# Kernel optimization log

Hardware: AMD Instinct MI355X
Metric: run time of the kernel (lower is better)

The kernel has to match this reference:

```python
import jax, jax.numpy as jnp
import numpy as np

B, T, NG, NP, DV = 256, 100, 4096, 512, 2


def setup_inputs() -> dict:
    key = jax.random.key(0)
    k = jax.random.split(key, 6)
    v = jax.random.normal(k[0], (B, T, DV), dtype=jnp.float32) * 0.1
    P0 = jax.random.uniform(k[1], (B, NP), dtype=jnp.float32)
    # Dense kernels (glorot-ish scale); recurrent kernel uniform(-0.02, 0.02) per the module
    W_enc = jax.random.normal(k[2], (NP, NG), dtype=jnp.float32) / np.sqrt(NP)
    W_in = jax.random.normal(k[3], (DV, NG), dtype=jnp.float32) / np.sqrt(DV)
    W_rec = (jax.random.uniform(k[4], (NG, NG), dtype=jnp.float32) * 2.0 - 1.0) * 0.02
    W_dec = jax.random.normal(k[5], (NG, NP), dtype=jnp.float32) / np.sqrt(NG)
    return {"v": v, "P0": P0, "W_enc": W_enc, "W_in": W_in, "W_rec": W_rec, "W_dec": W_dec}


def reference(v, P0, W_enc, W_in, W_rec, W_dec):
    # encoder: init hidden state from place-cell code P0  -> [B, Ng]
    h0 = P0 @ W_enc
    # Precompute input projection for all timesteps: [B, T, Ng] -> scan over T
    xW = jnp.einsum('btd,dg->btg', v, W_in)
    xW_t = jnp.swapaxes(xW, 0, 1)  # [T, B, Ng]

    def step(h, x):
        h_new = jax.nn.relu(x + h @ W_rec)
        return h_new, h_new

    _, g = jax.lax.scan(step, h0, xW_t)      # g: [T, B, Ng]
    g = jnp.swapaxes(g, 0, 1)                # [B, T, Ng]
    place_preds = jnp.einsum('btg,gp->btp', g, W_dec)  # [B, T, Np]
    return place_preds
```

## Files before the change

### kernel.cpp

```cpp
#include <hip/hip_runtime.h>
#include <hip/hip_bf16.h>

typedef __attribute__((ext_vector_type(8))) short bf16x8;
typedef __attribute__((ext_vector_type(4))) float f32x4;

#define MFMA __builtin_amdgcn_mfma_f32_16x16x32_bf16

__device__ __forceinline__ short f2bf(float f) {
    union { __hip_bfloat16 h; short s; } u;
    u.h = __float2bfloat16(f);
    return u.s;
}

__device__ __forceinline__ void gld_lds16(const void* g, void* l) {
    auto gp = (const __attribute__((address_space(1))) void*)(g);
    auto lp = (__attribute__((address_space(3))) void*)(l);
    __builtin_amdgcn_global_load_lds(gp, lp, 16, 0, 0);
}

__global__ __launch_bounds__(64) void cvt_tile(const float* __restrict__ in,
                                               __hip_bfloat16* __restrict__ out, int C) {
    const int cd32 = C >> 5;
    const int tile = blockIdx.x;
    const int r16 = tile / cd32, c32 = tile - r16 * cd32;
    const int l = threadIdx.x;
    const int row = (r16 << 4) + (l & 15);
    const int c0 = (c32 << 5) + ((l >> 4) << 3);
    const float* src = in + (size_t)row * C + c0;
    short o[8];
#pragma unroll
    for (int j = 0; j < 8; ++j) o[j] = f2bf(src[j]);
    *(bf16x8*)((char*)out + (size_t)tile * 1024 + (l << 4)) = *(bf16x8*)o;
}

__global__ __launch_bounds__(256) void tcvt256(const float* __restrict__ in,
                                               __hip_bfloat16* __restrict__ out,
                                               int N, int K) {
    __shared__ float tile[64][65];
    const int r0 = blockIdx.x << 6;
    const int c0 = blockIdx.y << 6;
    const int tid = threadIdx.x;
    const int row = tid >> 2, cq = tid & 3;
#pragma unroll
    for (int it = 0; it < 4; ++it) {
        int c4 = cq + (it << 2);
        float4 vv = *(const float4*)(in + (size_t)(r0 + row) * N + c0 + (c4 << 2));
        tile[row][(c4 << 2) + 0] = vv.x;
        tile[row][(c4 << 2) + 1] = vv.y;
        tile[row][(c4 << 2) + 2] = vv.z;
        tile[row][(c4 << 2) + 3] = vv.w;
    }
    __syncthreads();
    const int kd32 = K >> 5;
#pragma unroll
    for (int half = 0; half < 2; ++half) {
        int slot = tid + (half << 8);
        int ti = slot >> 6, l = slot & 63;
        int ci = ti & 3, ri = ti >> 2;
        short o[8];
#pragma unroll
        for (int j = 0; j < 8; ++j)
            o[j] = f2bf(tile[(ri << 5) + ((l >> 4) << 3) + j][(ci << 4) + (l & 15)]);
        size_t tidx = (size_t)((c0 >> 4) + ci) * kd32 + (r0 >> 5) + ri;
        *(bf16x8*)((char*)out + tidx * 1024 + (l << 4)) = *(bf16x8*)o;
    }
}

template <int MODE, int NW, int KC>
__global__ __launch_bounds__(NW * 64) void gemm_r(const __hip_bfloat16* __restrict__ A,
                                                  const __hip_bfloat16* __restrict__ B,
                                                  void* __restrict__ outp,
                                                  const float* __restrict__ v,
                                                  const float* __restrict__ Wi, int t) {
    constexpr int KD32 = KC * NW;
    __shared__ __align__(16) char lds[NW * 16384];
    const int id = blockIdx.x;
    const int xcd = id & 7, j = id >> 3;
    const int bn = (xcd << 3) + (j & 7);
    const int bm = j >> 3;
    const int tid = threadIdx.x, wv = tid >> 6, lane = tid & 63;
    char* myl = lds + (wv << 14);
    const int kw0 = wv * KC;
    const int bm4 = bm << 2, bn4 = bn << 2;

    constexpr size_t FSTR = (size_t)KD32 << 10;
    const char* pA = (const char*)A + (((size_t)(bm4 * KD32 + kw0)) << 10) + (lane << 4);
    const char* pB = (const char*)B + (((size_t)(bn4 * KD32 + kw0)) << 10) + (lane << 4);

    f32x4 acc[4][4] = {};
    bf16x8 A00, A01, A02, A03, A10, A11, A12, A13,
           A20, A21, A22, A23, A30, A31, A32, A33;
    bf16x8 B00, B01, B02, B03, B10, B11, B12, B13,
           B20, B21, B22, B23, B30, B31, B32, B33;

#define LOADG(S, KI)                                       \
    do {                                                   \
        const char* pa_ = pA + ((size_t)(KI) << 10);       \
        const char* pb_ = pB + ((size_t)(KI) << 10);       \
        A##S##0 = *(const bf16x8*)(pa_);                   \
        A##S##1 = *(const bf16x8*)(pa_ + FSTR);            \
        A##S##2 = *(const bf16x8*)(pa_ + 2 * FSTR);        \
        A##S##3 = *(const bf16x8*)(pa_ + 3 * FSTR);        \
        B##S##0 = *(const bf16x8*)(pb_);                   \
        B##S##1 = *(const bf16x8*)(pb_ + FSTR);            \
        B##S##2 = *(const bf16x8*)(pb_ + 2 * FSTR);        \
        B##S##3 = *(const bf16x8*)(pb_ + 3 * FSTR);        \
    } while (0)

#define COMPUTE(S)                                             \
    do {                                                       \
        acc[0][0] = MFMA(A##S##0, B##S##0, acc[0][0], 0, 0, 0);\
        acc[0][1] = MFMA(A##S##0, B##S##1, acc[0][1], 0, 0, 0);\
        acc[0][2] = MFMA(A##S##0, B##S##2, acc[0][2], 0, 0, 0);\
        acc[0][3] = MFMA(A##S##0, B##S##3, acc[0][3], 0, 0, 0);\
        acc[1][0] = MFMA(A##S##1, B##S##0, acc[1][0], 0, 0, 0);\
        acc[1][1] = MFMA(A##S##1, B##S##1, acc[1][1], 0, 0, 0);\
        acc[1][2] = MFMA(A##S##1, B##S##2, acc[1][2], 0, 0, 0);\
        acc[1][3] = MFMA(A##S##1, B##S##3, acc[1][3], 0, 0, 0);\
        acc[2][0] = MFMA(A##S##2, B##S##0, acc[2][0], 0, 0, 0);\
        acc[2][1] = MFMA(A##S##2, B##S##1, acc[2][1], 0, 0, 0);\
        acc[2][2] = MFMA(A##S##2, B##S##2, acc[2][2], 0, 0, 0);\
        acc[2][3] = MFMA(A##S##2, B##S##3, acc[2][3], 0, 0, 0);\
        acc[3][0] = MFMA(A##S##3, B##S##0, acc[3][0], 0, 0, 0);\
        acc[3][1] = MFMA(A##S##3, B##S##1, acc[3][1], 0, 0, 0);\
        acc[3][2] = MFMA(A##S##3, B##S##2, acc[3][2], 0, 0, 0);\
        acc[3][3] = MFMA(A##S##3, B##S##3, acc[3][3], 0, 0, 0);\
    } while (0)

#define ITER(S, SP, DOISS, KI)                  \
    do {                                        \
        if (DOISS) LOADG(SP, (KI) + 3);         \
        __builtin_amdgcn_sched_barrier(0);      \
        COMPUTE(S);                             \
        __builtin_amdgcn_sched_barrier(0);      \
    } while (0)

    LOADG(0, 0);
    __builtin_amdgcn_sched_barrier(0);
    LOADG(1, 1);
    __builtin_amdgcn_sched_barrier(0);
    LOADG(2, 2);
    __builtin_amdgcn_sched_barrier(0);

    int s = 0;
    for (; s + 4 < KC; s += 4) {
        ITER(0, 3, true, s + 0);
        ITER(1, 0, true, s + 1);
        ITER(2, 1, true, s + 2);
        ITER(3, 2, true, s + 3);
    }
    ITER(0, 3, true,  s + 0);
    ITER(1, 0, false, s + 1);
    ITER(2, 1, false, s + 2);
    ITER(3, 2, false, s + 3);

#undef ITER
#undef COMPUTE
#undef LOADG

#pragma unroll
    for (int f = 0; f < 4; ++f)
#pragma unroll
        for (int g = 0; g < 4; ++g)
            *(f32x4*)(myl + (((f << 2) + g) << 10) + (lane << 4)) = acc[f][g];
    __syncthreads();

    constexpr int FPW = 16 / NW;
    f32x4 fin[FPW];
#pragma unroll
    for (int q = 0; q < FPW; ++q) {
        const int fid = wv * FPW + q;
        f32x4 ssum = {};
#pragma unroll
        for (int w = 0; w < NW; ++w)
            ssum += *(const f32x4*)(lds + (w << 14) + (fid << 10) + (lane << 4));
        fin[q] = ssum;
    }

    char* O = (char*)outp;
#pragma unroll
    for (int q = 0; q < FPW; ++q) {
        const int fid = wv * FPW + q;
        const int fr = fid >> 2, g = fid & 3;
        const int rbase = (bm << 6) + (fr << 4) + ((lane >> 4) << 2);
        const int c = (bn << 6) + (g << 4) + (lane & 15);
#pragma unroll
        for (int j = 0; j < 4; ++j) {
            int r = rbase + j;
            float val = fin[q][j];
            if constexpr (MODE == 1) {
                float v0 = v[(size_t)(r * 100 + t) * 2 + 0];
                float v1 = v[(size_t)(r * 100 + t) * 2 + 1];
                val = fmaxf(val + v0 * Wi[c] + v1 * Wi[4096 + c], 0.0f);
            }
            size_t off = ((size_t)(r >> 4) * 128 + (c >> 5)) * 1024 +
                         ((size_t)((r & 15) + (((c >> 3) & 3) << 4)) << 4) +
                         ((c & 7) << 1);
            *(short*)(O + off) = f2bf(val);
        }
    }
}

__global__ __launch_bounds__(512) void gemm_dec(const __hip_bfloat16* __restrict__ G,
                                                const __hip_bfloat16* __restrict__ Wdt,
                                                float* __restrict__ out) {
    __shared__ __align__(16) char lds[65536];
    const int id = blockIdx.x;
    const int t = id >> 1, nh = id & 1;
    const int tid = threadIdx.x, wv = tid >> 6, lane = tid & 63;

    const char* pA = (const char*)G + (size_t)t * 2097152 +
                     ((size_t)(wv << 1) << 17) + (lane << 4);
    const char* pB = (const char*)Wdt + ((size_t)(nh << 4) << 17) + (lane << 4);

    f32x4 acc0[16] = {};
    f32x4 acc1[16] = {};
    bf16x8 A00, A01, A10, A11, A20, A21, A30, A31;

#define STAGE(SLOT, KI)                                                  \
    do {                                                                 \
        char* d_ = lds + ((SLOT) << 14);                                 \
        const char* b_ = pB + (((size_t)(wv << 1)) << 17) +              \
                         ((size_t)(KI) << 10);                           \
        gld_lds16(b_, d_ + ((wv << 1) << 10));                           \
        gld_lds16(b_ + (1 << 17), d_ + (((wv << 1) + 1) << 10));         \
    } while (0)

#define LOADA(S, KI)                                                     \
    do {                                                                 \
        const char* a_ = pA + ((size_t)(KI) << 10);                      \
        A##S##0 = *(const bf16x8*)(a_);                                  \
        A##S##1 = *(const bf16x8*)(a_ + (1 << 17));                      \
    } while (0)

#define COMPUTE(S)                                                       \
    do {                                                                 \
        const char* bb_ = lds + ((S) << 14) + (lane << 4);               \
        _Pragma("unroll") for (int f = 0; f < 16; ++f) {                 \
            bf16x8 b_ = *(const bf16x8*)(bb_ + (f << 10));               \
            acc0[f] = MFMA(A##S##0, b_, acc0[f], 0, 0, 0);               \
            acc1[f] = MFMA(A##S##1, b_, acc1[f], 0, 0, 0);               \
        }                                                                \
    } while (0)

#define ITER(S, SP, VM, DOISS, KI)                                 \
    do {                                                           \
        asm volatile("s_waitcnt vmcnt(%0)" ::"i"(VM) : "memory");  \
        __builtin_amdgcn_s_barrier();                              \
        __builtin_amdgcn_sched_barrier(0);                         \
        if (DOISS) {                                               \
            STAGE(SP, (KI) + 3);                                   \
            LOADA(SP, (KI) + 3);                                   \
        }                                                          \
        __builtin_amdgcn_sched_barrier(0);                         \
        COMPUTE(S);                                                \
    } while (0)

    STAGE(0, 0); LOADA(0, 0);
    __builtin_amdgcn_sched_barrier(0);
    STAGE(1, 1); LOADA(1, 1);
    __builtin_amdgcn_sched_barrier(0);
    STAGE(2, 2); LOADA(2, 2);
    __builtin_amdgcn_sched_barrier(0);

    int s = 0;
    for (; s + 4 < 128; s += 4) {
        ITER(0, 3, 8, true, s + 0);
        ITER(1, 0, 8, true, s + 1);
        ITER(2, 1, 8, true, s + 2);
        ITER(3, 2, 8, true, s + 3);
    }
    ITER(0, 3, 8, true,  s + 0);
    ITER(1, 0, 8, false, s + 1);
    ITER(2, 1, 4, false, s + 2);
    ITER(3, 2, 0, false, s + 3);

#undef ITER
#undef COMPUTE
#undef LOADA
#undef STAGE

    const int rb = (wv << 5) + ((lane >> 4) << 2);
    const int cb = (nh << 8) + (lane & 15);
#pragma unroll
    for (int f = 0; f < 16; ++f) {
        const int c = cb + (f << 4);
#pragma unroll
        for (int j = 0; j < 4; ++j) {
            int b0 = rb + j;
            int b1 = rb + 16 + j;
            out[((size_t)b0 * 100 + t) * 512 + c] = acc0[f][j];
            out[((size_t)b1 * 100 + t) * 512 + c] = acc1[f][j];
        }
    }
}

extern "C" void kernel_launch(void* const* d_in, const int* in_sizes, int n_in,
                              void* d_out, int out_size, void* d_ws, size_t ws_size,
                              hipStream_t stream) {
    const float* v     = (const float*)d_in[0];
    const float* P0    = (const float*)d_in[1];
    const float* W_enc = (const float*)d_in[2];
    const float* W_in  = (const float*)d_in[3];
    const float* W_rec = (const float*)d_in[4];
    const float* W_dec = (const float*)d_in[5];
    float* out = (float*)d_out;

    char* ws = (char*)d_ws;
    __hip_bfloat16* Wrt = (__hip_bfloat16*)(ws + 0);
    __hip_bfloat16* Wet = (__hip_bfloat16*)(ws + 33554432);
    __hip_bfloat16* Wdt = (__hip_bfloat16*)(ws + 37748736);
    __hip_bfloat16* P0t = (__hip_bfloat16*)(ws + 41943040);
    __hip_bfloat16* h0  = (__hip_bfloat16*)(ws + 42205184);
    __hip_bfloat16* G   = (__hip_bfloat16*)(ws + 44302336);

    tcvt256<<<dim3(64, 64), 256, 0, stream>>>(W_rec, Wrt, 4096, 4096);
    tcvt256<<<dim3(8, 64), 256, 0, stream>>>(W_enc, Wet, 4096, 512);
    tcvt256<<<dim3(64, 8), 256, 0, stream>>>(W_dec, Wdt, 512, 4096);
    cvt_tile<<<256, 64, 0, stream>>>(P0, P0t, 512);

    gemm_r<0, 4, 4><<<256, 256, 0, stream>>>(P0t, Wet, (void*)h0, nullptr, nullptr, 0);

    for (int t = 0; t < 100; ++t) {
        const __hip_bfloat16* hprev = (t == 0) ? h0 : (G + (size_t)(t - 1) * 1048576);
        gemm_r<1, 4, 32><<<256, 256, 0, stream>>>(hprev, Wrt,
                                                  (void*)(G + (size_t)t * 1048576), v, W_in, t);
    }

    gemm_dec<<<200, 512, 0, stream>>>(G, Wdt, out);
}
```

Before: 1.468 ms.

## Replace split-K recurrent GEMM with M/N wave tiling, removing LDS reduction

The per-step recurrent GEMM kernel now assigns each of the four waves a 32x32 sub-tile over the full K range instead of splitting K across waves and reducing partial 64x64 tiles through shared memory. This removes the LDS store, barrier and cross-wave sum in the epilogue. In exchange each wave runs a longer K loop with only four independent accumulators, and the block issues twice as many global fragment loads, reducing MFMA latency hiding and raising cache traffic.

```diff
diff --git a/kernel.cpp b/kernel.cpp
--- a/kernel.cpp
+++ b/kernel.cpp
@@ -66,65 +66,45 @@
     }
 }
 
-template <int MODE, int NW, int KC>
-__global__ __launch_bounds__(NW * 64) void gemm_r(const __hip_bfloat16* __restrict__ A,
-                                                  const __hip_bfloat16* __restrict__ B,
-                                                  void* __restrict__ outp,
-                                                  const float* __restrict__ v,
-                                                  const float* __restrict__ Wi, int t) {
-    constexpr int KD32 = KC * NW;
-    __shared__ __align__(16) char lds[NW * 16384];
+template <int MODE, int KD32>
+__global__ __launch_bounds__(256) void gemm_mn(const __hip_bfloat16* __restrict__ A,
+                                               const __hip_bfloat16* __restrict__ B,
+                                               void* __restrict__ outp,
+                                               const float* __restrict__ v,
+                                               const float* __restrict__ Wi, int t) {
     const int id = blockIdx.x;
     const int xcd = id & 7, j = id >> 3;
     const int bn = (xcd << 3) + (j & 7);
     const int bm = j >> 3;
     const int tid = threadIdx.x, wv = tid >> 6, lane = tid & 63;
-    char* myl = lds + (wv << 14);
-    const int kw0 = wv * KC;
-    const int bm4 = bm << 2, bn4 = bn << 2;
+    const int wr = wv >> 1, wc = wv & 1;
 
     constexpr size_t FSTR = (size_t)KD32 << 10;
-    const char* pA = (const char*)A + (((size_t)(bm4 * KD32 + kw0)) << 10) + (lane << 4);
-    const char* pB = (const char*)B + (((size_t)(bn4 * KD32 + kw0)) << 10) + (lane << 4);
-
-    f32x4 acc[4][4] = {};
-    bf16x8 A00, A01, A02, A03, A10, A11, A12, A13,
-           A20, A21, A22, A23, A30, A31, A32, A33;
-    bf16x8 B00, B01, B02, B03, B10, B11, B12, B13,
-           B20, B21, B22, B23, B30, B31, B32, B33;
-
-#define LOADG(S, KI)                                       \
-    do {                                                   \
-        const char* pa_ = pA + ((size_t)(KI) << 10);       \
-        const char* pb_ = pB + ((size_t)(KI) << 10);       \
-        A##S##0 = *(const bf16x8*)(pa_);                   \
-        A##S##1 = *(const bf16x8*)(pa_ + FSTR);            \
-        A##S##2 = *(const bf16x8*)(pa_ + 2 * FSTR);        \
-        A##S##3 = *(const bf16x8*)(pa_ + 3 * FSTR);        \
-        B##S##0 = *(const bf16x8*)(pb_);                   \
-        B##S##1 = *(const bf16x8*)(pb_ + FSTR);            \
-        B##S##2 = *(const bf16x8*)(pb_ + 2 * FSTR);        \
-        B##S##3 = *(const bf16x8*)(pb_ + 3 * FSTR);        \
-    } while (0)
-
-#define COMPUTE(S)                                             \
-    do {                                                       \
-        acc[0][0] = MFMA(A##S##0, B##S##0, acc[0][0], 0, 0, 0);\
-        acc[0][1] = MFMA(A##S##0, B##S##1, acc[0][1], 0, 0, 0);\
-        acc[0][2] = MFMA(A##S##0, B##S##2, acc[0][2], 0, 0, 0);\
-        acc[0][3] = MFMA(A##S##0, B##S##3, acc[0][3], 0, 0, 0);\
-        acc[1][0] = MFMA(A##S##1, B##S##0, acc[1][0], 0, 0, 0);\
-        acc[1][1] = MFMA(A##S##1, B##S##1, acc[1][1], 0, 0, 0);\
-        acc[1][2] = MFMA(A##S##1, B##S##2, acc[1][2], 0, 0, 0);\
-        acc[1][3] = MFMA(A##S##1, B##S##3, acc[1][3], 0, 0, 0);\
-        acc[2][0] = MFMA(A##S##2, B##S##0, acc[2][0], 0, 0, 0);\
-        acc[2][1] = MFMA(A##S##2, B##S##1, acc[2][1], 0, 0, 0);\
-        acc[2][2] = MFMA(A##S##2, B##S##2, acc[2][2], 0, 0, 0);\
-        acc[2][3] = MFMA(A##S##2, B##S##3, acc[2][3], 0, 0, 0);\
-        acc[3][0] = MFMA(A##S##3, B##S##0, acc[3][0], 0, 0, 0);\
-        acc[3][1] = MFMA(A##S##3, B##S##1, acc[3][1], 0, 0, 0);\
-        acc[3][2] = MFMA(A##S##3, B##S##2, acc[3][2], 0, 0, 0);\
-        acc[3][3] = MFMA(A##S##3, B##S##3, acc[3][3], 0, 0, 0);\
+    const char* pA = (const char*)A +
+                     ((size_t)(((bm << 2) + (wr << 1)) * KD32) << 10) + (lane << 4);
+    const char* pB = (const char*)B +
+                     ((size_t)(((bn << 2) + (wc << 1)) * KD32) << 10) + (lane << 4);
+
+    f32x4 acc00 = {}, acc01 = {}, acc10 = {}, acc11 = {};
+    bf16x8 A00, A01, A10, A11, A20, A21, A30, A31;
+    bf16x8 B00, B01, B10, B11, B20, B21, B30, B31;
+
+#define LOADG(S, KI)                                  \
+    do {                                              \
+        const char* pa_ = pA + ((size_t)(KI) << 10);  \
+        const char* pb_ = pB + ((size_t)(KI) << 10);  \
+        A##S##0 = *(const bf16x8*)(pa_);              \
+        A##S##1 = *(const bf16x8*)(pa_ + FSTR);       \
+        B##S##0 = *(const bf16x8*)(pb_);              \
+        B##S##1 = *(const bf16x8*)(pb_ + FSTR);       \
+    } while (0)
+
+#define COMPUTE(S)                                     \
+    do {                                               \
+        acc00 = MFMA(A##S##0, B##S##0, acc00, 0, 0, 0);\
+        acc01 = MFMA(A##S##0, B##S##1, acc01, 0, 0, 0);\
+        acc10 = MFMA(A##S##1, B##S##0, acc10, 0, 0, 0);\
+        acc11 = MFMA(A##S##1, B##S##1, acc11, 0, 0, 0);\
     } while (0)
 
 #define ITER(S, SP, DOISS, KI)                  \
@@ -143,7 +123,7 @@
     __builtin_amdgcn_sched_barrier(0);
 
     int s = 0;
-    for (; s + 4 < KC; s += 4) {
+    for (; s + 4 < KD32; s += 4) {
         ITER(0, 3, true, s + 0);
         ITER(1, 0, true, s + 1);
         ITER(2, 1, true, s + 2);
@@ -158,47 +138,39 @@
 #undef COMPUTE
 #undef LOADG
 
-#pragma unroll
-    for (int f = 0; f < 4; ++f)
-#pragma unroll
-        for (int g = 0; g < 4; ++g)
-            *(f32x4*)(myl + (((f << 2) + g) << 10) + (lane << 4)) = acc[f][g];
-    __syncthreads();
-
-    constexpr int FPW = 16 / NW;
-    f32x4 fin[FPW];
-#pragma unroll
-    for (int q = 0; q < FPW; ++q) {
-        const int fid = wv * FPW + q;
-        f32x4 ssum = {};
-#pragma unroll
-        for (int w = 0; w < NW; ++w)
-            ssum += *(const f32x4*)(lds + (w << 14) + (fid << 10) + (lane << 4));
-        fin[q] = ssum;
-    }
-
+    float av[2][2][4];
+#pragma unroll
+    for (int q = 0; q < 4; ++q) {
+        av[0][0][q] = acc00[q]; av[0][1][q] = acc01[q];
+        av[1][0][q] = acc10[q]; av[1][1][q] = acc11[q];
+    }
+
+    const int rb = (bm << 6) + (wr << 5) + ((lane >> 4) << 2);
+    const int cb = (bn << 6) + (wc << 5) + (lane & 15);
     char* O = (char*)outp;
 #pragma unroll
-    for (int q = 0; q < FPW; ++q) {
-        const int fid = wv * FPW + q;
-        const int fr = fid >> 2, g = fid & 3;
-        const int rbase = (bm << 6) + (fr << 4) + ((lane >> 4) << 2);
-        const int c = (bn << 6) + (g << 4) + (lane & 15);
+    for (int f = 0; f < 2; ++f)
 #pragma unroll
         for (int j = 0; j < 4; ++j) {
-            int r = rbase + j;
-            float val = fin[q][j];
+            int r = rb + (f << 4) + j;
+            float v0 = 0.f, v1 = 0.f;
             if constexpr (MODE == 1) {
-                float v0 = v[(size_t)(r * 100 + t) * 2 + 0];
-                float v1 = v[(size_t)(r * 100 + t) * 2 + 1];
-                val = fmaxf(val + v0 * Wi[c] + v1 * Wi[4096 + c], 0.0f);
+                v0 = v[(size_t)(r * 100 + t) * 2 + 0];
+                v1 = v[(size_t)(r * 100 + t) * 2 + 1];
             }
-            size_t off = ((size_t)(r >> 4) * 128 + (c >> 5)) * 1024 +
-                         ((size_t)((r & 15) + (((c >> 3) & 3) << 4)) << 4) +
-                         ((c & 7) << 1);
-            *(short*)(O + off) = f2bf(val);
+#pragma unroll
+            for (int g = 0; g < 2; ++g) {
+                int c = cb + (g << 4);
+                float val = av[f][g][j];
+                if constexpr (MODE == 1) {
+                    val = fmaxf(val + v0 * Wi[c] + v1 * Wi[4096 + c], 0.0f);
+                }
+                size_t off = ((size_t)(r >> 4) * 128 + (c >> 5)) * 1024 +
+                             ((size_t)((r & 15) + (((c >> 3) & 3) << 4)) << 4) +
+                             ((c & 7) << 1);
+                *(short*)(O + off) = f2bf(val);
+            }
         }
-    }
 }
 
 __global__ __launch_bounds__(512) void gemm_dec(const __hip_bfloat16* __restrict__ G,
@@ -319,12 +291,12 @@
     tcvt256<<<dim3(64, 8), 256, 0, stream>>>(W_dec, Wdt, 512, 4096);
     cvt_tile<<<256, 64, 0, stream>>>(P0, P0t, 512);
 
-    gemm_r<0, 4, 4><<<256, 256, 0, stream>>>(P0t, Wet, (void*)h0, nullptr, nullptr, 0);
+    gemm_mn<0, 16><<<256, 256, 0, stream>>>(P0t, Wet, (void*)h0, nullptr, nullptr, 0);
 
     for (int t = 0; t < 100; ++t) {
         const __hip_bfloat16* hprev = (t == 0) ? h0 : (G + (size_t)(t - 1) * 1048576);
-        gemm_r<1, 4, 32><<<256, 256, 0, stream>>>(hprev, Wrt,
-                                                  (void*)(G + (size_t)t * 1048576), v, W_in, t);
+        gemm_mn<1, 128><<<256, 256, 0, stream>>>(hprev, Wrt,
+                                                 (void*)(G + (size_t)t * 1048576), v, W_in, t);
     }
 
     gemm_dec<<<200, 512, 0, stream>>>(G, Wdt, out);
```

New measurement: 1.893 ms. 29.0% more time.
